# Optimization experiments

Hardware: AMD Instinct MI355X
Metric: run time of the kernel (lower is better)

The kernel has to match this reference:

```python
import jax, jax.numpy as jnp
import numpy as np

B, T, C_IN, H, K1, NUM_CLASSES = 64, 4096, 64, 96, 128, 109


def conv1d(x, w, b, stride, pad):
    # x: [B, C, T], w: [O, I, K]
    y = jax.lax.conv_general_dilated(x, w, (stride,), [(pad, pad)],
                                     dimension_numbers=('NCH', 'OIH', 'NCH'))
    return y + b[None, :, None]


def bn1d(x, g, b, m, v, eps=1e-5):
    # eval-mode BatchNorm1d over channel dim of [B, C, T]
    scale = g / jnp.sqrt(v + eps)
    return (x - m[None, :, None]) * scale[None, :, None] + b[None, :, None]


def slstm(x, wx, wh, bias):
    # sLSTM block with exponential gating + stabilizer state m (xLSTM paper).
    # x: [B, T, H]; wx, wh: [4H, H] (gate order: z, i, f, o); bias: [4H]
    Bn, Tn, Hn = x.shape
    pre = jnp.einsum('bth,gh->btg', x, wx) + bias  # [B, T, 4H], input part precomputed

    def step(carry, px):
        h, c, n, m = carry
        g = px + h @ wh.T  # [B, 4H]
        zp, ip, fp, op = jnp.split(g, 4, axis=-1)
        z = jnp.tanh(zp)
        o = jax.nn.sigmoid(op)
        m_new = jnp.maximum(fp + m, ip)          # stabilizer
        i = jnp.exp(ip - m_new)
        f = jnp.exp(fp + m - m_new)
        c_new = f * c + i * z
        n_new = f * n + i
        h_new = o * (c_new / jnp.maximum(n_new, 1.0))
        return (h_new, c_new, n_new, m_new), h_new

    z0 = jnp.zeros((Bn, Hn), x.dtype)
    _, ys = jax.lax.scan(step, (z0, z0, z0, z0), pre.transpose(1, 0, 2))
    return ys.transpose(1, 0, 2)  # [B, T, H]


def setup_inputs():
    key = jax.random.key(0)
    ks = jax.random.split(key, 10)

    def rn(k, shape, s=0.05):
        return jax.random.normal(k, shape, jnp.float32) * s

    z = lambda n: jnp.zeros((n,), jnp.float32)
    o = lambda n: jnp.ones((n,), jnp.float32)
    return {
        'x': jax.random.normal(ks[0], (B, T, C_IN), jnp.float32),
        'conv1_w': rn(ks[1], (K1, C_IN, 7)), 'conv1_b': z(K1),
        'bn1_g': o(K1), 'bn1_b': z(K1), 'bn1_m': z(K1), 'bn1_v': o(K1),
        'conv2_w': rn(ks[2], (H, K1, 3)), 'conv2_b': z(H),
        'bn2_g': o(H), 'bn2_b': z(H), 'bn2_m': z(H), 'bn2_v': o(H),
        'res_w': rn(ks[3], (H, K1, 1)), 'res_b': z(H),
        'bnr_g': o(H), 'bnr_b': z(H), 'bnr_m': z(H), 'bnr_v': o(H),
        'slstm_wx': rn(ks[4], (4 * H, H)), 'slstm_wh': rn(ks[5], (4 * H, H)), 'slstm_bias': z(4 * H),
        'fc1_w': rn(ks[6], (128, H)), 'fc1_b': z(128),
        'fc2_w': rn(ks[7], (NUM_CLASSES, 128)), 'fc2_b': z(NUM_CLASSES),
    }


def reference(x, conv1_w, conv1_b, bn1_g, bn1_b, bn1_m, bn1_v,
              conv2_w, conv2_b, bn2_g, bn2_b, bn2_m, bn2_v,
              res_w, res_b, bnr_g, bnr_b, bnr_m, bnr_v,
              slstm_wx, slstm_wh, slstm_bias,
              fc1_w, fc1_b, fc2_w, fc2_b):
    xt = x.transpose(0, 2, 1)  # [B, C_IN, T]
    out = jax.nn.relu(bn1d(conv1d(xt, conv1_w, conv1_b, 1, 3), bn1_g, bn1_b, bn1_m, bn1_v))  # [B, 128, T]
    residual = bn1d(conv1d(out, res_w, res_b, 4, 0), bnr_g, bnr_b, bnr_m, bnr_v)  # [B, H, T//4]
    out = jax.nn.relu(bn1d(conv1d(out, conv2_w, conv2_b, 4, 1), bn2_g, bn2_b, bn2_m, bn2_v)) + residual
    seq = out.transpose(0, 2, 1)  # [B, T//4, H]
    h = slstm(seq, slstm_wx, slstm_wh, slstm_bias)
    pooled = h.mean(axis=1)  # AdaptiveAvgPool1d(1) over time -> [B, H]
    z1 = jax.nn.relu(pooled @ fc1_w.T + fc1_b)
    return z1 @ fc2_w.T + fc2_b  # [B, NUM_CLASSES]
```

## Files before the change

### kernel.cpp

```cpp
#include <hip/hip_runtime.h>
#include <hip/hip_bf16.h>
#include <math.h>

typedef unsigned short u16;
typedef short bf16x8 __attribute__((ext_vector_type(8)));
typedef float f32x4 __attribute__((ext_vector_type(4)));

#define Bz 64
#define Tt 4096
#define Cin 64
#define K1c 128
#define Hh 96
#define T2 1024
#define G4 384
#define NC 109

#define MFMA16(a, b, c) __builtin_amdgcn_mfma_f32_16x16x32_bf16(a, b, c, 0, 0, 0)

__device__ __forceinline__ float bf2f(u16 v) {
  union { unsigned int u; float f; } x; x.u = ((unsigned int)v) << 16; return x.f;
}
__device__ __forceinline__ u16 f2bf(float f) {
  union { unsigned int u; float f; } x; x.f = f;
  unsigned int u = x.u;
  unsigned int r = u + 0x7fff + ((u >> 16) & 1);
  return (u16)(r >> 16);
}

__device__ __forceinline__ float gate_scale(int g) {
  const float L2E = 1.44269504f;
  return (g == 0) ? 2.f * L2E : L2E;
}

__global__ void k_prep(const float* __restrict__ w1, const float* __restrict__ cb1,
                       const float* __restrict__ g1, const float* __restrict__ b1,
                       const float* __restrict__ m1, const float* __restrict__ v1,
                       const float* __restrict__ w2, const float* __restrict__ cb2,
                       const float* __restrict__ g2, const float* __restrict__ b2,
                       const float* __restrict__ m2, const float* __restrict__ v2,
                       const float* __restrict__ wr, const float* __restrict__ cbr,
                       const float* __restrict__ gr, const float* __restrict__ br,
                       const float* __restrict__ mr, const float* __restrict__ vr,
                       const float* __restrict__ wx, const float* __restrict__ sbia,
                       const float* __restrict__ wh,
                       u16* __restrict__ w1b, u16* __restrict__ w2b,
                       u16* __restrict__ wrb, u16* __restrict__ wxb,
                       float* __restrict__ bperm, u16* __restrict__ whb,
                       float* __restrict__ al1, float* __restrict__ be1,
                       float* __restrict__ al2, float* __restrict__ be2,
                       float* __restrict__ alr, float* __restrict__ ber)
{
  int tid = blockIdx.x * blockDim.x + threadIdx.x;
  int nth = gridDim.x * blockDim.x;
  for (int idx = tid; idx < 128 * 448; idx += nth) {
    int o = idx / 448, k = idx % 448;
    int kt = k >> 6, c = k & 63;
    w1b[idx] = f2bf(w1[(o * 64 + c) * 7 + kt]);
  }
  for (int idx = tid; idx < 96 * 384; idx += nth) {
    int o = idx / 384, k = idx % 384;
    int kk = k >> 7, c = k & 127;
    w2b[idx] = f2bf(w2[(o * 128 + c) * 3 + kk]);
  }
  for (int idx = tid; idx < 96 * 128; idx += nth) {
    wrb[idx] = f2bf(wr[idx]);
  }
  for (int idx = tid; idx < 384 * 96; idx += nth) {
    int row = idx / 96, k = idx % 96;
    int ch = row >> 2, g = row & 3;
    wxb[idx] = f2bf(wx[((size_t)(g * 96 + ch)) * 96 + k] * gate_scale(g));
  }
  for (int c = tid; c < 384; c += nth) {
    int ch = c >> 2, g = c & 3;
    bperm[c] = sbia[g * 96 + ch] * gate_scale(g);
  }
  for (int idx = tid; idx < 384 * 96; idx += nth) {
    int row = idx / 96, k = idx % 96;
    int ch = row >> 2, g = row & 3;
    whb[idx] = f2bf(wh[((size_t)(g * 96 + ch)) * 96 + k] * gate_scale(g));
  }
  for (int o = tid; o < 128; o += nth) {
    float a = g1[o] / sqrtf(v1[o] + 1e-5f);
    al1[o] = a; be1[o] = b1[o] + (cb1[o] - m1[o]) * a;
  }
  for (int o = tid; o < 96; o += nth) {
    float a = g2[o] / sqrtf(v2[o] + 1e-5f);
    al2[o] = a; be2[o] = b2[o] + (cb2[o] - m2[o]) * a;
    float ar = gr[o] / sqrtf(vr[o] + 1e-5f);
    alr[o] = ar; ber[o] = br[o] + (cbr[o] - mr[o]) * ar;
  }
}

__launch_bounds__(256, 2)
__global__ void k_conv1(const float* __restrict__ x, const u16* __restrict__ w1b,
                        const float* __restrict__ al1, const float* __restrict__ be1,
                        u16* __restrict__ out1)
{
  __shared__ __align__(16) u16 xs[134 * 72];
  int tid = threadIdx.x;
  int b = blockIdx.y;
  int t0 = blockIdx.x * 128;
  const float* xb = x + (size_t)b * Tt * Cin;

  for (int idx = tid; idx < 134 * 16; idx += 256) {
    int row = idx >> 4, c4 = (idx & 15) << 2;
    int gt = t0 - 3 + row;
    float4 v = make_float4(0.f, 0.f, 0.f, 0.f);
    if (gt >= 0 && gt < Tt) v = *(const float4*)(xb + (size_t)gt * 64 + c4);
    ushort4 s;
    s.x = f2bf(v.x); s.y = f2bf(v.y); s.z = f2bf(v.z); s.w = f2bf(v.w);
    *(ushort4*)(xs + row * 72 + c4) = s;
  }
  __syncthreads();

  int l = tid & 63;
  int wid = tid >> 6;
  int wm = wid >> 1, wn = wid & 1;
  int lr = l & 15, g = l >> 4;

  f32x4 acc[4][4];
#pragma unroll
  for (int i = 0; i < 4; i++)
#pragma unroll
    for (int j = 0; j < 4; j++) acc[i][j] = (f32x4){0.f, 0.f, 0.f, 0.f};

  const u16* wbase = w1b + (size_t)(wn * 64 + lr) * 448;

  for (int s = 0; s < 14; ++s) {
    int kt = s >> 1;
    int cofs = ((s & 1) << 5) + (g << 3);
    const u16* xrow = xs + (wm * 64 + lr + kt) * 72 + cofs;
    bf16x8 a0 = *(const bf16x8*)(xrow);
    bf16x8 a1 = *(const bf16x8*)(xrow + 16 * 72);
    bf16x8 a2 = *(const bf16x8*)(xrow + 32 * 72);
    bf16x8 a3 = *(const bf16x8*)(xrow + 48 * 72);
    int ko = (s << 5) + (g << 3);
    bf16x8 b0 = *(const bf16x8*)(wbase + ko);
    bf16x8 b1 = *(const bf16x8*)(wbase + 16 * 448 + ko);
    bf16x8 b2 = *(const bf16x8*)(wbase + 32 * 448 + ko);
    bf16x8 b3 = *(const bf16x8*)(wbase + 48 * 448 + ko);
    acc[0][0] = MFMA16(a0, b0, acc[0][0]);
    acc[0][1] = MFMA16(a0, b1, acc[0][1]);
    acc[0][2] = MFMA16(a0, b2, acc[0][2]);
    acc[0][3] = MFMA16(a0, b3, acc[0][3]);
    acc[1][0] = MFMA16(a1, b0, acc[1][0]);
    acc[1][1] = MFMA16(a1, b1, acc[1][1]);
    acc[1][2] = MFMA16(a1, b2, acc[1][2]);
    acc[1][3] = MFMA16(a1, b3, acc[1][3]);
    acc[2][0] = MFMA16(a2, b0, acc[2][0]);
    acc[2][1] = MFMA16(a2, b1, acc[2][1]);
    acc[2][2] = MFMA16(a2, b2, acc[2][2]);
    acc[2][3] = MFMA16(a2, b3, acc[2][3]);
    acc[3][0] = MFMA16(a3, b0, acc[3][0]);
    acc[3][1] = MFMA16(a3, b1, acc[3][1]);
    acc[3][2] = MFMA16(a3, b2, acc[3][2]);
    acc[3][3] = MFMA16(a3, b3, acc[3][3]);
  }

  int colb = wn * 64 + lr;
  int rowb = t0 + wm * 64 + (l >> 4) * 4;
#pragma unroll
  for (int nf = 0; nf < 4; nf++) {
    int col = colb + nf * 16;
    float A = al1[col], Bt = be1[col];
#pragma unroll
    for (int mf = 0; mf < 4; mf++) {
      int row = rowb + mf * 16;
#pragma unroll
      for (int r = 0; r < 4; r++) {
        float v = acc[mf][nf][r];
        v = fmaxf(v * A + Bt, 0.f);
        out1[((size_t)b * Tt + row + r) * 128 + col] = f2bf(v);
      }
    }
  }
}

__launch_bounds__(256, 4)
__global__ void k_conv2(const u16* __restrict__ out1, const u16* __restrict__ w2b,
                        const u16* __restrict__ wrb,
                        const float* __restrict__ al2, const float* __restrict__ be2,
                        const float* __restrict__ alr, const float* __restrict__ ber,
                        u16* __restrict__ seqb)
{
  int tid = threadIdx.x;
  int b = blockIdx.y;
  int t20 = blockIdx.x * 64;
  int l = tid & 63;
  int wid = tid >> 6;
  int wm = wid >> 1, wn = wid & 1;
  int lr = l & 15, g = l >> 4;

  f32x4 acc[2][3], accr[2][3];
#pragma unroll
  for (int i = 0; i < 2; i++)
#pragma unroll
    for (int j = 0; j < 3; j++) {
      acc[i][j] = (f32x4){0.f, 0.f, 0.f, 0.f};
      accr[i][j] = (f32x4){0.f, 0.f, 0.f, 0.f};
    }

  const u16* ob = out1 + (size_t)b * Tt * 128;
  int colb = wn * 48 + lr;

#pragma unroll
  for (int f = 0; f < 12; f++) {
    int kk = f >> 2;
    int c = ((f & 3) << 5) + (g << 3);
    bf16x8 a[2];
#pragma unroll
    for (int mf = 0; mf < 2; mf++) {
      int t2 = t20 + wm * 32 + mf * 16 + lr;
      int gt = 4 * t2 + kk - 1;
      if (gt >= 0)
        a[mf] = *(const bf16x8*)(ob + (size_t)gt * 128 + c);
      else
        a[mf] = (bf16x8){0, 0, 0, 0, 0, 0, 0, 0};
    }
#pragma unroll
    for (int nf = 0; nf < 3; nf++) {
      int col = colb + nf * 16;
      bf16x8 bb = *(const bf16x8*)(w2b + (size_t)col * 384 + (f << 5) + (g << 3));
      acc[0][nf] = MFMA16(a[0], bb, acc[0][nf]);
      acc[1][nf] = MFMA16(a[1], bb, acc[1][nf]);
    }
    if (kk == 1) {
#pragma unroll
      for (int nf = 0; nf < 3; nf++) {
        int col = colb + nf * 16;
        bf16x8 br = *(const bf16x8*)(wrb + (size_t)col * 128 + ((f & 3) << 5) + (g << 3));
        accr[0][nf] = MFMA16(a[0], br, accr[0][nf]);
        accr[1][nf] = MFMA16(a[1], br, accr[1][nf]);
      }
    }
  }

  int rowb = t20 + wm * 32 + (l >> 4) * 4;
#pragma unroll
  for (int nf = 0; nf < 3; nf++) {
    int col = colb + nf * 16;
    float A = al2[col], Bt = be2[col];
    float Ar = alr[col], Br = ber[col];
#pragma unroll
    for (int mf = 0; mf < 2; mf++) {
      int row = rowb + mf * 16;
#pragma unroll
      for (int r = 0; r < 4; r++) {
        float v = fmaxf(acc[mf][nf][r] * A + Bt, 0.f) + accr[mf][nf][r] * Ar + Br;
        seqb[((size_t)b * T2 + row + r) * 96 + col] = f2bf(v);
      }
    }
  }
}

__launch_bounds__(512, 1)
__global__ void k_slstm(const u16* __restrict__ seqb, const u16* __restrict__ whb,
                        const u16* __restrict__ wxb, const float* __restrict__ bperm,
                        float* __restrict__ hsum)
{
  __shared__ __align__(16) float pxring[32][388];
  __shared__ __align__(16) u16 hbufB[2][96];
  int tid = threadIdx.x;
  int b = blockIdx.x;
  int w = tid >> 6;
  int l = tid & 63;
  int grp = l >> 4, lr = l & 15;

  if (w < 4) {
    bf16x8 af[6][3];
#pragma unroll
    for (int m = 0; m < 6; m++) {
      const u16* wrow = whb + (size_t)(96 * w + 16 * m + lr) * 96 + grp * 8;
#pragma unroll
      for (int kt = 0; kt < 3; kt++) af[m][kt] = *(const bf16x8*)(wrow + kt * 32);
    }
    bool gl = (lr < 6);
    int ch = 24 * w + 4 * lr + grp;
    float cS = 0.f, nS = 0.f, mS = 0.f, hs = 0.f;
    if (tid < 96) hbufB[0][tid] = 0;
    __syncthreads();
    __syncthreads();
    f32x4 pxA[6], pxB[6];
#pragma unroll
    for (int m = 0; m < 6; m++)
      pxA[m] = *(const f32x4*)(&pxring[0][96 * w + 16 * m + 4 * grp]);

    int p = 0;
#define CONS_STEP(PXC, PXN, TT)                                                \
  {                                                                            \
    __builtin_amdgcn_s_setprio(1);                                             \
    const u16* hb_ = hbufB[p] + grp * 8;                                       \
    bf16x8 h0_ = *(const bf16x8*)(hb_);                                        \
    bf16x8 h1_ = *(const bf16x8*)(hb_ + 32);                                   \
    bf16x8 h2_ = *(const bf16x8*)(hb_ + 64);                                   \
    const float* pxs_ = &pxring[((TT) + 1) & 31][96 * w];                      \
    _Pragma("unroll")                                                          \
    for (int m = 0; m < 6; m++)                                                \
      PXN[m] = *(const f32x4*)(pxs_ + 16 * m + 4 * grp);                       \
    f32x4 acc_[6];                                                             \
    _Pragma("unroll")                                                          \
    for (int m = 0; m < 6; m++) {                                              \
      acc_[m] = MFMA16(af[m][0], h0_, PXC[m]);                                 \
      acc_[m] = MFMA16(af[m][1], h1_, acc_[m]);                                \
      acc_[m] = MFMA16(af[m][2], h2_, acc_[m]);                                \
    }                                                                          \
    f32x4 x01_ = (lr & 1) ? acc_[1] : acc_[0];                                 \
    f32x4 x23_ = (lr & 1) ? acc_[3] : acc_[2];                                 \
    f32x4 x45_ = (lr & 1) ? acc_[5] : acc_[4];                                 \
    f32x4 y0_ = (lr & 2) ? x23_ : x01_;                                        \
    f32x4 pa_ = (lr & 4) ? x45_ : y0_;                                         \
    if (gl) {                                                                  \
      float zp_ = pa_[0], ip_ = pa_[1], fp_ = pa_[2], op_ = pa_[3];            \
      float zc_ = fminf(fmaxf(zp_, -86.f), 86.f);                              \
      float ez_ = exp2f(zc_);                                                  \
      float z_ = 1.f - 2.f * __builtin_amdgcn_rcpf(ez_ + 1.f);                 \
      float oc_ = fminf(fmaxf(op_, -60.f), 60.f);                              \
      float o_ = __builtin_amdgcn_rcpf(1.f + exp2f(-oc_));                     \
      float mn_ = fmaxf(fp_ + mS, ip_);                                        \
      float iv_ = exp2f(ip_ - mn_);                                            \
      float fv_ = exp2f(fp_ + mS - mn_);                                       \
      cS = fv_ * cS + iv_ * z_;                                                \
      nS = fv_ * nS + iv_;                                                     \
      mS = mn_;                                                                \
      float h_ = o_ * cS * __builtin_amdgcn_rcpf(fmaxf(nS, 1.f));              \
      hs += h_;                                                                \
      hbufB[p ^ 1][ch] = f2bf(h_);                                             \
    }                                                                          \
    __builtin_amdgcn_s_setprio(0);                                             \
    __syncthreads();                                                           \
    p ^= 1;                                                                    \
  }

    for (int t = 0; t < T2; t += 2) {
      CONS_STEP(pxA, pxB, t);
      CONS_STEP(pxB, pxA, t + 1);
    }
#undef CONS_STEP
    if (gl) hsum[b * 96 + ch] = hs * (1.f / 1024.f);
  } else {
    int pw = w - 4;
    bf16x8 wf[6][3];
#pragma unroll
    for (int m = 0; m < 6; m++) {
      const u16* xrow = wxb + (size_t)(96 * pw + 16 * m + lr) * 96 + grp * 8;
#pragma unroll
      for (int kt = 0; kt < 3; kt++) wf[m][kt] = *(const bf16x8*)(xrow + kt * 32);
    }
    f32x4 bias6[6];
#pragma unroll
    for (int m = 0; m < 6; m++)
      bias6[m] = *(const f32x4*)(bperm + 96 * pw + 16 * m + 4 * grp);

    const u16* sqB = seqb + (size_t)b * T2 * 96 + grp * 8;

    __syncthreads();
    {
      const u16* sp_ = sqB + (size_t)lr * 96;
      bf16x8 s0 = *(const bf16x8*)(sp_);
      bf16x8 s1 = *(const bf16x8*)(sp_ + 32);
      bf16x8 s2 = *(const bf16x8*)(sp_ + 64);
      f32x4 pc[6];
#pragma unroll
      for (int m = 0; m < 6; m++) {
        pc[m] = MFMA16(wf[m][0], s0, bias6[m]);
        pc[m] = MFMA16(wf[m][1], s1, pc[m]);
        pc[m] = MFMA16(wf[m][2], s2, pc[m]);
      }
#pragma unroll
      for (int m = 0; m < 6; m++)
        *(f32x4*)(&pxring[lr][96 * pw + 16 * m + 4 * grp]) = pc[m];
    }
    bf16x8 s0, s1, s2;
    {
      int ts = 16 + lr; if (ts > T2 - 1) ts = T2 - 1;
      const u16* sp_ = sqB + (size_t)ts * 96;
      s0 = *(const bf16x8*)(sp_);
      s1 = *(const bf16x8*)(sp_ + 32);
      s2 = *(const bf16x8*)(sp_ + 64);
    }
    __syncthreads();

    for (int t = 0; t < T2; t++) {
      if (((t & 15) == 0) && (t + 16 < T2)) {
        f32x4 pacc[6];
#pragma unroll
        for (int m = 0; m < 6; m++) {
          pacc[m] = MFMA16(wf[m][0], s0, bias6[m]);
          pacc[m] = MFMA16(wf[m][1], s1, pacc[m]);
          pacc[m] = MFMA16(wf[m][2], s2, pacc[m]);
        }
        int slot = (t + 16 + lr) & 31;
#pragma unroll
        for (int m = 0; m < 6; m++)
          *(f32x4*)(&pxring[slot][96 * pw + 16 * m + 4 * grp]) = pacc[m];
        int ts = t + 32 + lr; if (ts > T2 - 1) ts = T2 - 1;
        const u16* sp_ = sqB + (size_t)ts * 96;
        s0 = *(const bf16x8*)(sp_);
        s1 = *(const bf16x8*)(sp_ + 32);
        s2 = *(const bf16x8*)(sp_ + 64);
      }
      __syncthreads();
    }
  }
}

__launch_bounds__(128)
__global__ void k_head(const float* __restrict__ hsum, const float* __restrict__ fc1w,
                       const float* __restrict__ fc1b, const float* __restrict__ fc2w,
                       const float* __restrict__ fc2b, float* __restrict__ out)
{
  __shared__ float p[96];
  __shared__ float z1[128];
  int tid = threadIdx.x, b = blockIdx.x;
  if (tid < 96) p[tid] = hsum[b * 96 + tid];
  __syncthreads();
  {
    float a = fc1b[tid];
    const float* wr = fc1w + tid * 96;
    for (int h = 0; h < 96; h++) a += p[h] * wr[h];
    z1[tid] = fmaxf(a, 0.f);
  }
  __syncthreads();
  if (tid < NC) {
    float a = fc2b[tid];
    const float* wr = fc2w + tid * 128;
    for (int j = 0; j < 128; j++) a += z1[j] * wr[j];
    out[b * NC + tid] = a;
  }
}

extern "C" void kernel_launch(void* const* d_in, const int* in_sizes, int n_in,
                              void* d_out, int out_size, void* d_ws, size_t ws_size,
                              hipStream_t stream)
{
  const float* x    = (const float*)d_in[0];
  const float* w1   = (const float*)d_in[1];
  const float* cb1  = (const float*)d_in[2];
  const float* g1   = (const float*)d_in[3];
  const float* b1   = (const float*)d_in[4];
  const float* m1   = (const float*)d_in[5];
  const float* v1   = (const float*)d_in[6];
  const float* w2   = (const float*)d_in[7];
  const float* cb2  = (const float*)d_in[8];
  const float* g2   = (const float*)d_in[9];
  const float* b2   = (const float*)d_in[10];
  const float* m2   = (const float*)d_in[11];
  const float* v2   = (const float*)d_in[12];
  const float* wr   = (const float*)d_in[13];
  const float* cbr  = (const float*)d_in[14];
  const float* gr   = (const float*)d_in[15];
  const float* br   = (const float*)d_in[16];
  const float* mr   = (const float*)d_in[17];
  const float* vr   = (const float*)d_in[18];
  const float* wx   = (const float*)d_in[19];
  const float* wh   = (const float*)d_in[20];
  const float* sbia = (const float*)d_in[21];
  const float* fc1w = (const float*)d_in[22];
  const float* fc1b = (const float*)d_in[23];
  const float* fc2w = (const float*)d_in[24];
  const float* fc2b = (const float*)d_in[25];

  char* ws = (char*)d_ws;
  size_t off = 0;
  auto alloc = [&](size_t bytes) -> void* {
    void* p = (void*)(ws + off);
    off = (off + bytes + 255) & ~((size_t)255);
    return p;
  };
  u16*   out1 = (u16*)  alloc((size_t)Bz * Tt * K1c * 2);
  u16*   seqb = (u16*)  alloc((size_t)Bz * T2 * Hh * 2);
  u16*   w1b  = (u16*)  alloc(448 * 128 * 2);
  u16*   w2b  = (u16*)  alloc(96 * 384 * 2);
  u16*   wrb  = (u16*)  alloc(96 * 128 * 2);
  u16*   wxb  = (u16*)  alloc(384 * 96 * 2);
  float* bperm= (float*)alloc(384 * 4);
  u16*   whb  = (u16*)  alloc(384 * 96 * 2);
  float* al1  = (float*)alloc(128 * 4);
  float* be1  = (float*)alloc(128 * 4);
  float* al2  = (float*)alloc(96 * 4);
  float* be2  = (float*)alloc(96 * 4);
  float* alr  = (float*)alloc(96 * 4);
  float* ber  = (float*)alloc(96 * 4);
  float* hsum = (float*)alloc((size_t)Bz * Hh * 4);
  (void)ws_size; (void)in_sizes; (void)n_in; (void)out_size;

  k_prep<<<dim3(224), dim3(256), 0, stream>>>(
      w1, cb1, g1, b1, m1, v1, w2, cb2, g2, b2, m2, v2,
      wr, cbr, gr, br, mr, vr, wx, sbia, wh,
      w1b, w2b, wrb, wxb, bperm, whb, al1, be1, al2, be2, alr, ber);

  k_conv1<<<dim3(Tt / 128, Bz), dim3(256), 0, stream>>>(x, w1b, al1, be1, out1);

  k_conv2<<<dim3(T2 / 64, Bz), dim3(256), 0, stream>>>(out1, w2b, wrb, al2, be2, alr, ber, seqb);

  k_slstm<<<dim3(Bz), dim3(512), 0, stream>>>(seqb, whb, wxb, bperm, hsum);

  k_head<<<dim3(Bz), dim3(128), 0, stream>>>(hsum, fc1w, fc1b, fc2w, fc2b, (float*)d_out);
}
```

Before: 512.8 us.

## Split sLSTM recurrence across all eight waves with inline input projection

The sLSTM kernel no longer splits waves into four consumers running the recurrence and four producers precomputing the input projection. All eight waves now run the recurrence, each owning 48 gate rows (3 MFMA tiles instead of 6). Each wave also computes its own slice of the input projection into the ring buffer every 16 steps. This halves the per-step recurrent MFMA work on each wave to shorten the serial step latency, at the cost of a periodic projection burst inside the critical loop and more register pressure from holding both weight sets.

```diff
diff --git a/kernel.cpp b/kernel.cpp
--- a/kernel.cpp
+++ b/kernel.cpp
@@ -266,26 +266,60 @@
   int l = tid & 63;
   int grp = l >> 4, lr = l & 15;
 
-  if (w < 4) {
-    bf16x8 af[6][3];
-#pragma unroll
-    for (int m = 0; m < 6; m++) {
-      const u16* wrow = whb + (size_t)(96 * w + 16 * m + lr) * 96 + grp * 8;
-#pragma unroll
-      for (int kt = 0; kt < 3; kt++) af[m][kt] = *(const bf16x8*)(wrow + kt * 32);
-    }
-    bool gl = (lr < 6);
-    int ch = 24 * w + 4 * lr + grp;
-    float cS = 0.f, nS = 0.f, mS = 0.f, hs = 0.f;
-    if (tid < 96) hbufB[0][tid] = 0;
-    __syncthreads();
-    __syncthreads();
-    f32x4 pxA[6], pxB[6];
-#pragma unroll
-    for (int m = 0; m < 6; m++)
-      pxA[m] = *(const f32x4*)(&pxring[0][96 * w + 16 * m + 4 * grp]);
-
-    int p = 0;
+  bf16x8 af[3][3], wf[3][3];
+#pragma unroll
+  for (int m = 0; m < 3; m++) {
+    const u16* wrow = whb + (size_t)(48 * w + 16 * m + lr) * 96 + grp * 8;
+    const u16* xrow = wxb + (size_t)(48 * w + 16 * m + lr) * 96 + grp * 8;
+#pragma unroll
+    for (int kt = 0; kt < 3; kt++) {
+      af[m][kt] = *(const bf16x8*)(wrow + kt * 32);
+      wf[m][kt] = *(const bf16x8*)(xrow + kt * 32);
+    }
+  }
+  f32x4 bias3[3];
+#pragma unroll
+  for (int m = 0; m < 3; m++)
+    bias3[m] = *(const f32x4*)(bperm + 48 * w + 16 * m + 4 * grp);
+
+  bool gl = (lr < 3);
+  int ch = 12 * w + 4 * lr + grp;
+  const u16* sqB = seqb + (size_t)b * T2 * 96 + grp * 8;
+
+  {
+    const u16* sp_ = sqB + (size_t)lr * 96;
+    bf16x8 q0 = *(const bf16x8*)(sp_);
+    bf16x8 q1 = *(const bf16x8*)(sp_ + 32);
+    bf16x8 q2 = *(const bf16x8*)(sp_ + 64);
+    f32x4 pc[3];
+#pragma unroll
+    for (int m = 0; m < 3; m++) {
+      pc[m] = MFMA16(wf[m][0], q0, bias3[m]);
+      pc[m] = MFMA16(wf[m][1], q1, pc[m]);
+      pc[m] = MFMA16(wf[m][2], q2, pc[m]);
+    }
+#pragma unroll
+    for (int m = 0; m < 3; m++)
+      *(f32x4*)(&pxring[lr][48 * w + 16 * m + 4 * grp]) = pc[m];
+  }
+  bf16x8 s0, s1, s2;
+  {
+    int ts = 16 + lr; if (ts > T2 - 1) ts = T2 - 1;
+    const u16* sp_ = sqB + (size_t)ts * 96;
+    s0 = *(const bf16x8*)(sp_);
+    s1 = *(const bf16x8*)(sp_ + 32);
+    s2 = *(const bf16x8*)(sp_ + 64);
+  }
+  if (tid < 96) hbufB[0][tid] = 0;
+  float cS = 0.f, nS = 0.f, mS = 0.f, hs = 0.f;
+  __syncthreads();
+
+  f32x4 pxA[3], pxB[3];
+#pragma unroll
+  for (int m = 0; m < 3; m++)
+    pxA[m] = *(const f32x4*)(&pxring[0][48 * w + 16 * m + 4 * grp]);
+
+  int p = 0;
 #define CONS_STEP(PXC, PXN, TT)                                                \
   {                                                                            \
     __builtin_amdgcn_s_setprio(1);                                             \
@@ -293,22 +327,37 @@
     bf16x8 h0_ = *(const bf16x8*)(hb_);                                        \
     bf16x8 h1_ = *(const bf16x8*)(hb_ + 32);                                   \
     bf16x8 h2_ = *(const bf16x8*)(hb_ + 64);                                   \
-    const float* pxs_ = &pxring[((TT) + 1) & 31][96 * w];                      \
+    const float* pxs_ = &pxring[((TT) + 1) & 31][48 * w];                      \
     _Pragma("unroll")                                                          \
-    for (int m = 0; m < 6; m++)                                                \
+    for (int m = 0; m < 3; m++)                                                \
       PXN[m] = *(const f32x4*)(pxs_ + 16 * m + 4 * grp);                       \
-    f32x4 acc_[6];                                                             \
+    if ((((TT) & 15) == 0) && ((TT) + 16 < T2)) {                              \
+      f32x4 pacc_[3];                                                          \
+      _Pragma("unroll")                                                        \
+      for (int m = 0; m < 3; m++) {                                            \
+        pacc_[m] = MFMA16(wf[m][0], s0, bias3[m]);                             \
+        pacc_[m] = MFMA16(wf[m][1], s1, pacc_[m]);                             \
+        pacc_[m] = MFMA16(wf[m][2], s2, pacc_[m]);                             \
+      }                                                                        \
+      int slot_ = ((TT) + 16 + lr) & 31;                                       \
+      _Pragma("unroll")                                                        \
+      for (int m = 0; m < 3; m++)                                              \
+        *(f32x4*)(&pxring[slot_][48 * w + 16 * m + 4 * grp]) = pacc_[m];       \
+      int ts_ = (TT) + 32 + lr; if (ts_ > T2 - 1) ts_ = T2 - 1;                \
+      const u16* sp_ = sqB + (size_t)ts_ * 96;                                 \
+      s0 = *(const bf16x8*)(sp_);                                              \
+      s1 = *(const bf16x8*)(sp_ + 32);                                         \
+      s2 = *(const bf16x8*)(sp_ + 64);                                         \
+    }                                                                          \
+    f32x4 acc_[3];                                                             \
     _Pragma("unroll")                                                          \
-    for (int m = 0; m < 6; m++) {                                              \
+    for (int m = 0; m < 3; m++) {                                              \
       acc_[m] = MFMA16(af[m][0], h0_, PXC[m]);                                 \
       acc_[m] = MFMA16(af[m][1], h1_, acc_[m]);                                \
       acc_[m] = MFMA16(af[m][2], h2_, acc_[m]);                                \
     }                                                                          \
     f32x4 x01_ = (lr & 1) ? acc_[1] : acc_[0];                                 \
-    f32x4 x23_ = (lr & 1) ? acc_[3] : acc_[2];                                 \
-    f32x4 x45_ = (lr & 1) ? acc_[5] : acc_[4];                                 \
-    f32x4 y0_ = (lr & 2) ? x23_ : x01_;                                        \
-    f32x4 pa_ = (lr & 4) ? x45_ : y0_;                                         \
+    f32x4 pa_ = (lr & 2) ? acc_[2] : x01_;                                     \
     if (gl) {                                                                  \
       float zp_ = pa_[0], ip_ = pa_[1], fp_ = pa_[2], op_ = pa_[3];            \
       float zc_ = fminf(fmaxf(zp_, -86.f), 86.f);                              \
@@ -331,77 +380,12 @@
     p ^= 1;                                                                    \
   }
 
-    for (int t = 0; t < T2; t += 2) {
-      CONS_STEP(pxA, pxB, t);
-      CONS_STEP(pxB, pxA, t + 1);
-    }
+  for (int t = 0; t < T2; t += 2) {
+    CONS_STEP(pxA, pxB, t);
+    CONS_STEP(pxB, pxA, t + 1);
+  }
 #undef CONS_STEP
-    if (gl) hsum[b * 96 + ch] = hs * (1.f / 1024.f);
-  } else {
-    int pw = w - 4;
-    bf16x8 wf[6][3];
-#pragma unroll
-    for (int m = 0; m < 6; m++) {
-      const u16* xrow = wxb + (size_t)(96 * pw + 16 * m + lr) * 96 + grp * 8;
-#pragma unroll
-      for (int kt = 0; kt < 3; kt++) wf[m][kt] = *(const bf16x8*)(xrow + kt * 32);
-    }
-    f32x4 bias6[6];
-#pragma unroll
-    for (int m = 0; m < 6; m++)
-      bias6[m] = *(const f32x4*)(bperm + 96 * pw + 16 * m + 4 * grp);
-
-    const u16* sqB = seqb + (size_t)b * T2 * 96 + grp * 8;
-
-    __syncthreads();
-    {
-      const u16* sp_ = sqB + (size_t)lr * 96;
-      bf16x8 s0 = *(const bf16x8*)(sp_);
-      bf16x8 s1 = *(const bf16x8*)(sp_ + 32);
-      bf16x8 s2 = *(const bf16x8*)(sp_ + 64);
-      f32x4 pc[6];
-#pragma unroll
-      for (int m = 0; m < 6; m++) {
-        pc[m] = MFMA16(wf[m][0], s0, bias6[m]);
-        pc[m] = MFMA16(wf[m][1], s1, pc[m]);
-        pc[m] = MFMA16(wf[m][2], s2, pc[m]);
-      }
-#pragma unroll
-      for (int m = 0; m < 6; m++)
-        *(f32x4*)(&pxring[lr][96 * pw + 16 * m + 4 * grp]) = pc[m];
-    }
-    bf16x8 s0, s1, s2;
-    {
-      int ts = 16 + lr; if (ts > T2 - 1) ts = T2 - 1;
-      const u16* sp_ = sqB + (size_t)ts * 96;
-      s0 = *(const bf16x8*)(sp_);
-      s1 = *(const bf16x8*)(sp_ + 32);
-      s2 = *(const bf16x8*)(sp_ + 64);
-    }
-    __syncthreads();
-
-    for (int t = 0; t < T2; t++) {
-      if (((t & 15) == 0) && (t + 16 < T2)) {
-        f32x4 pacc[6];
-#pragma unroll
-        for (int m = 0; m < 6; m++) {
-          pacc[m] = MFMA16(wf[m][0], s0, bias6[m]);
-          pacc[m] = MFMA16(wf[m][1], s1, pacc[m]);
-          pacc[m] = MFMA16(wf[m][2], s2, pacc[m]);
-        }
-        int slot = (t + 16 + lr) & 31;
-#pragma unroll
-        for (int m = 0; m < 6; m++)
-          *(f32x4*)(&pxring[slot][96 * pw + 16 * m + 4 * grp]) = pacc[m];
-        int ts = t + 32 + lr; if (ts > T2 - 1) ts = T2 - 1;
-        const u16* sp_ = sqB + (size_t)ts * 96;
-        s0 = *(const bf16x8*)(sp_);
-        s1 = *(const bf16x8*)(sp_ + 32);
-        s2 = *(const bf16x8*)(sp_ + 64);
-      }
-      __syncthreads();
-    }
-  }
+  if (gl) hsum[b * 96 + ch] = hs * (1.f / 1024.f);
 }
 
 __launch_bounds__(128)
```

Measured after the change: 543.3 us. 6.0% more time.
